# Optimization experiments

Hardware: AMD Instinct MI355X
Metric: run time of the kernel (lower is better)

## Reference

```python
import jax, jax.numpy as jnp
import numpy as np

N_NODES = 100000
N_EDGES = 3200000
G_EDGES = 1600000
D_FEAT = 256
K_CLUSTERS = 16
COLLAPSE_REG = 0.1


def setup_inputs() -> dict:
    key = jax.random.key(0)
    ks = jax.random.split(key, 12)
    inp = {
        'features': jax.random.normal(ks[0], (N_NODES, D_FEAT), dtype=jnp.float32),
        'W': jax.random.normal(ks[1], (D_FEAT, K_CLUSTERS), dtype=jnp.float32) / np.sqrt(D_FEAT),
        'b': jnp.zeros((K_CLUSTERS,), dtype=jnp.float32),
        'adj_src': jax.random.randint(ks[2], (N_EDGES,), 0, N_NODES, dtype=jnp.int32),
        'adj_dst': jax.random.randint(ks[3], (N_EDGES,), 0, N_NODES, dtype=jnp.int32),
        'adj_val': jax.random.uniform(ks[4], (N_EDGES,), dtype=jnp.float32),
        'g1_src': jax.random.randint(ks[5], (G_EDGES,), 0, N_NODES, dtype=jnp.int32),
        'g1_dst': jax.random.randint(ks[6], (G_EDGES,), 0, N_NODES, dtype=jnp.int32),
        'g1_val': jax.random.uniform(ks[7], (G_EDGES,), dtype=jnp.float32),
        'g2_src': jax.random.randint(ks[8], (G_EDGES,), 0, N_NODES, dtype=jnp.int32),
        'g2_dst': jax.random.randint(ks[9], (G_EDGES,), 0, N_NODES, dtype=jnp.int32),
        'g2_val': jax.random.uniform(ks[10], (G_EDGES,), dtype=jnp.float32),
        'lamda': 1,
    }
    return inp


def _spmm(src, dst, val, X, n):
    # (sparse A) @ X where A[src, dst] = val : out[i] = sum_j A[i,j] X[j]
    return jax.ops.segment_sum(val[:, None] * X[dst], src, num_segments=n)


def _col_degrees(src, dst, val, n):
    # tf.sparse.reduce_sum(A, axis=0): column sums
    return jax.ops.segment_sum(val, dst, num_segments=n)


def reference(features, W, b, adj_src, adj_dst, adj_val,
              g1_src, g1_dst, g1_val, g2_src, g2_dst, g2_val, lamda):
    n = features.shape[0]
    k = W.shape[1]
    # soft cluster assignments  [n, k]
    S = jax.nn.softmax(features @ W + b, axis=1)
    cluster_sizes = jnp.sum(S, axis=0)            # [k]
    S_pool = S / cluster_sizes                    # [n, k]

    # full-graph modularity
    deg = _col_degrees(adj_src, adj_dst, adj_val, n)  # [n]
    m = jnp.sum(deg)                                  # total edge weight
    AS = _spmm(adj_src, adj_dst, adj_val, S, n)       # [n, k]
    graph_pooled = AS.T @ S                           # [k, k]
    dS = deg @ S                                      # [k] = S^T deg
    normalizer = jnp.outer(dS, dS) / 2.0 / m          # [k, k]
    spectral_loss = -jnp.trace(graph_pooled - normalizer) / 2.0 / m

    # per-group modularity Q_g
    def group_Q(src, dst, val):
        gdeg = _col_degrees(src, dst, val, n)
        gm = jnp.sum(gdeg)
        safe_gm = jnp.where(gm > 0, gm, 1.0)
        gAS = _spmm(src, dst, val, S, n)
        g_pooled = gAS.T @ S
        gdS = gdeg @ S
        g_norm = jnp.outer(gdS, gdS) / 2.0 / safe_gm
        Qg = jnp.trace(g_pooled - g_norm) / 2.0 / m
        return jnp.where(gm > 0, Qg, 0.0), gm

    Q1, m1 = group_Q(g1_src, g1_dst, g1_val)
    Q2, m2 = group_Q(g2_src, g2_dst, g2_val)
    Q_min = jnp.minimum(Q1, Q2)
    g_edges_mean = (m1 + m2) / 2.0
    edge_ratio = m / (g_edges_mean + 1e-8)
    fairness_loss = edge_ratio * (-Q_min)

    collapse_loss = (jnp.linalg.norm(cluster_sizes) / n) * jnp.sqrt(jnp.float32(k)) - 1.0

    total_loss = spectral_loss + lamda * fairness_loss + COLLAPSE_REG * collapse_loss

    features_pooled = jax.nn.selu(S_pool.T @ features)  # [k, d]
    return features_pooled, S, total_loss
```

## Files before the change

### kernel.cpp

```cpp
#include <hip/hip_runtime.h>
#include <hip/hip_fp16.h>
#include <cstddef>


#define G1_MAX   1024
#define EGRID    2048
#define OFF_E    ((size_t)G1_MAX * 4112)
#define OFF_R    (OFF_E + (size_t)3 * 18 * EGRID)
#define OFF_G    (OFF_R + 4112)
#define OFF_H    (OFF_G + 64)

__global__ void __launch_bounds__(256)
k_rows(const float* __restrict__ F, const float* __restrict__ W,
       const float* __restrict__ b, float* __restrict__ S_out,
       __half* __restrict__ S_h, float* __restrict__ ws_P, int n, int n_tiles)
{
    __shared__ float Wt[16][260];
    __shared__ float rows[16][260];
    __shared__ float S_lds[16][17];
    __shared__ float cs_red[256];

    const int t = threadIdx.x;

    for (int idx = t; idx < 4096; idx += 256)
        Wt[idx & 15][idx >> 4] = W[idx];

    const float bk = b[t & 15];
    const int rl = t >> 4;
    const int kl = t & 15;
    const int kp = t & 15;
    const int cp = t >> 4;

    float4 P0 = {0,0,0,0}, P1 = {0,0,0,0}, P2 = {0,0,0,0}, P3 = {0,0,0,0};
    float cs_acc = 0.f;
    __syncthreads();

    for (int tile = blockIdx.x; tile < n_tiles; tile += gridDim.x) {
        const int row0 = tile << 4;
        const float4* F4 = (const float4*)(F + (size_t)row0 * 256);
        #pragma unroll
        for (int q = 0; q < 4; ++q) {
            int idx = t + (q << 8);
            int r = idx >> 6, dc = idx & 63;
            float4 v = {0.f, 0.f, 0.f, 0.f};
            if (row0 + r < n) v = F4[idx];
            *(float4*)&rows[r][dc << 2] = v;
        }
        __syncthreads();

        float acc = 0.f;
        #pragma unroll 8
        for (int dd = 0; dd < 64; ++dd) {
            float4 f4 = *(const float4*)&rows[rl][dd << 2];
            float4 w4 = *(const float4*)&Wt[kl][dd << 2];
            acc = fmaf(f4.x, w4.x, acc);
            acc = fmaf(f4.y, w4.y, acc);
            acc = fmaf(f4.z, w4.z, acc);
            acc = fmaf(f4.w, w4.w, acc);
        }
        acc += bk;

        float mx = acc;
        #pragma unroll
        for (int o = 8; o; o >>= 1) mx = fmaxf(mx, __shfl_xor(mx, o, 16));
        float ev = __expf(acc - mx);
        float sm = ev;
        #pragma unroll
        for (int o = 8; o; o >>= 1) sm += __shfl_xor(sm, o, 16);
        float sval = ev / sm;

        const bool valid = (row0 + rl) < n;
        if (valid) {
            S_out[(((size_t)(row0 + rl)) << 4) + kl] = sval;
            S_h[(((size_t)(row0 + rl)) << 4) + kl] = __float2half(sval);
            cs_acc += sval;
        }
        S_lds[rl][kl] = valid ? sval : 0.f;
        __syncthreads();

        #pragma unroll 4
        for (int r = 0; r < 16; ++r) {
            float sv = S_lds[r][kp];
            const float* rp = &rows[r][cp << 4];
            float4 f0 = *(const float4*)&rp[0];
            float4 f1 = *(const float4*)&rp[4];
            float4 f2 = *(const float4*)&rp[8];
            float4 f3 = *(const float4*)&rp[12];
            P0.x = fmaf(sv, f0.x, P0.x); P0.y = fmaf(sv, f0.y, P0.y);
            P0.z = fmaf(sv, f0.z, P0.z); P0.w = fmaf(sv, f0.w, P0.w);
            P1.x = fmaf(sv, f1.x, P1.x); P1.y = fmaf(sv, f1.y, P1.y);
            P1.z = fmaf(sv, f1.z, P1.z); P1.w = fmaf(sv, f1.w, P1.w);
            P2.x = fmaf(sv, f2.x, P2.x); P2.y = fmaf(sv, f2.y, P2.y);
            P2.z = fmaf(sv, f2.z, P2.z); P2.w = fmaf(sv, f2.w, P2.w);
            P3.x = fmaf(sv, f3.x, P3.x); P3.y = fmaf(sv, f3.y, P3.y);
            P3.z = fmaf(sv, f3.z, P3.z); P3.w = fmaf(sv, f3.w, P3.w);
        }
        __syncthreads();
    }

    {
        float* dst = ws_P + (size_t)blockIdx.x * 4112 + kp * 256 + (cp << 4);
        *(float4*)&dst[0]  = P0;
        *(float4*)&dst[4]  = P1;
        *(float4*)&dst[8]  = P2;
        *(float4*)&dst[12] = P3;
    }
    cs_red[t] = cs_acc;
    __syncthreads();
    if (t < 16) {
        float ssum = 0.f;
        #pragma unroll
        for (int i = 0; i < 16; ++i) ssum += cs_red[t + (i << 4)];
        ws_P[(size_t)blockIdx.x * 4112 + 4096 + t] = ssum;
    }
}

#define NSEG 16
__global__ void __launch_bounds__(256)
k_reduce(const float* __restrict__ ws_P, float* __restrict__ ws_red, int nb)
{
    const int seg  = blockIdx.x & (NSEG - 1);
    const int jblk = blockIdx.x / NSEG;
    const int idx  = jblk * 256 + threadIdx.x;
    if (idx >= 4112) return;
    const int chunk = (nb + NSEG - 1) / NSEG;
    const int b0 = seg * chunk;
    const int b1 = min(nb, b0 + chunk);
    float s = 0.f;
    for (int bb = b0; bb < b1; ++bb)
        s += ws_P[(size_t)bb * 4112 + idx];
    atomicAdd(&ws_red[idx], s);
}

__global__ void __launch_bounds__(256)
k_edges_all(const int* __restrict__ src0, const int* __restrict__ dst0,
            const float* __restrict__ val0, int n0,
            const int* __restrict__ src1, const int* __restrict__ dst1,
            const float* __restrict__ val1, int n1,
            const int* __restrict__ src2, const int* __restrict__ dst2,
            const float* __restrict__ val2, int n2,
            const __half* __restrict__ S_h, float* __restrict__ ws_e,
            int b0, int b1)
{
    int g, bb, nblk;
    const int* src; const int* dst; const float* val; int nE;
    if ((int)blockIdx.x < b0)      { g = 0; bb = blockIdx.x;          nblk = b0; src = src0; dst = dst0; val = val0; nE = n0; }
    else if ((int)blockIdx.x < b1) { g = 1; bb = blockIdx.x - b0;     nblk = b1 - b0; src = src1; dst = dst1; val = val1; nE = n1; }
    else                           { g = 2; bb = blockIdx.x - b1;     nblk = gridDim.x - b1; src = src2; dst = dst2; val = val2; nE = n2; }

    float m_acc = 0.f, tr_acc = 0.f;
    float gds[16];
    #pragma unroll
    for (int k = 0; k < 16; ++k) gds[k] = 0.f;

    const int nv = nE >> 2;
    const int stride = nblk * 256;
    for (int i = bb * 256 + threadIdx.x; i < nv; i += stride) {
        int4   s4 = ((const int4*)src)[i];
        int4   d4 = ((const int4*)dst)[i];
        float4 v4 = ((const float4*)val)[i];
        #pragma unroll
        for (int e = 0; e < 4; ++e) {
            int   si = (&s4.x)[e];
            int   di = (&d4.x)[e];
            float v  = (&v4.x)[e];
            uint4 sa = *(const uint4*)(S_h + ((size_t)si << 4));
            uint4 sb = *(const uint4*)(S_h + ((size_t)si << 4) + 8);
            uint4 da = *(const uint4*)(S_h + ((size_t)di << 4));
            uint4 db = *(const uint4*)(S_h + ((size_t)di << 4) + 8);
            float dot = 0.f;
            float dv[16];
            #pragma unroll
            for (int j = 0; j < 4; ++j) {
                float2 as = __half22float2(*(const __half2*)(&(&sa.x)[j]));
                float2 ad = __half22float2(*(const __half2*)(&(&da.x)[j]));
                float2 bs = __half22float2(*(const __half2*)(&(&sb.x)[j]));
                float2 bd = __half22float2(*(const __half2*)(&(&db.x)[j]));
                dot = fmaf(as.x, ad.x, dot); dot = fmaf(as.y, ad.y, dot);
                dot = fmaf(bs.x, bd.x, dot); dot = fmaf(bs.y, bd.y, dot);
                dv[2*j]     = ad.x; dv[2*j + 1] = ad.y;
                dv[8 + 2*j] = bd.x; dv[9 + 2*j] = bd.y;
            }
            m_acc += v;
            tr_acc = fmaf(v, dot, tr_acc);
            #pragma unroll
            for (int k = 0; k < 16; ++k) gds[k] = fmaf(v, dv[k], gds[k]);
        }
    }

    #pragma unroll
    for (int o = 32; o; o >>= 1) {
        m_acc  += __shfl_xor(m_acc, o);
        tr_acc += __shfl_xor(tr_acc, o);
        #pragma unroll
        for (int k = 0; k < 16; ++k) gds[k] += __shfl_xor(gds[k], o);
    }
    __shared__ float wred[4][18];
    const int wid = threadIdx.x >> 6, lane = threadIdx.x & 63;
    if (lane == 0) {
        wred[wid][0] = m_acc; wred[wid][1] = tr_acc;
        #pragma unroll
        for (int k = 0; k < 16; ++k) wred[wid][2 + k] = gds[k];
    }
    __syncthreads();
    if (threadIdx.x < 18) {
        float s = wred[0][threadIdx.x] + wred[1][threadIdx.x]
                + wred[2][threadIdx.x] + wred[3][threadIdx.x];
        ws_e[(size_t)g * 18 * EGRID + (size_t)threadIdx.x * EGRID + bb] = s;
    }
}

__global__ void __launch_bounds__(256)
k_ereduce(const float* __restrict__ ws_e, float* __restrict__ G54,
          int g0, int g1, int g2)
{
    const int p = blockIdx.x;
    const int g = p / 18, slot = p % 18;
    int grids[3] = {g0, g1, g2};
    const int gb = grids[g];
    const float* base = ws_e + (size_t)g * 18 * EGRID + (size_t)slot * EGRID;

    const int t = threadIdx.x;
    float s = 0.f;
    for (int bb = t; bb < gb; bb += 256) s += base[bb];
    #pragma unroll
    for (int o = 32; o; o >>= 1) s += __shfl_xor(s, o);

    __shared__ float wr[4];
    if ((t & 63) == 0) wr[t >> 6] = s;
    __syncthreads();
    if (t == 0) G54[p] = wr[0] + wr[1] + wr[2] + wr[3];
}

__global__ void __launch_bounds__(256)
k_final(const float* __restrict__ ws_red, const float* __restrict__ G54,
        const void* __restrict__ lamda_ptr, float* __restrict__ out, int n)
{
    __shared__ float G[54];
    const int t = threadIdx.x;
    if (t < 54) G[t] = G54[t];
    __syncthreads();

    const float* P  = ws_red;
    const float* cs = ws_red + 4096;

    const float scale = 1.0507009873554805f;
    const float alpha = 1.6732632423543772f;
    for (int idx = t; idx < 4096; idx += 256) {
        int k = idx >> 8;
        float x = P[idx] / cs[k];
        float y = x > 0.f ? scale * x : scale * alpha * (expf(x) - 1.f);
        out[idx] = y;
    }

    if (t == 0) {
        int   li = *(const int*)lamda_ptr;
        float lf = *(const float*)lamda_ptr;
        float lamda = (li > -100000 && li < 100000) ? (float)li : lf;

        float m = G[0], trA = G[1];
        float ds2 = 0.f;
        for (int k = 0; k < 16; ++k) ds2 += G[2 + k] * G[2 + k];
        float spectral = -(trA - ds2 / (2.f * m)) / (2.f * m);

        float Q[2], gm[2];
        for (int g = 0; g < 2; ++g) {
            const float* Gg = G + 18 * (g + 1);
            float mg = Gg[0], trg = Gg[1];
            float gds2 = 0.f;
            for (int k = 0; k < 16; ++k) gds2 += Gg[2 + k] * Gg[2 + k];
            float safe = mg > 0.f ? mg : 1.f;
            float q = (trg - gds2 / (2.f * safe)) / (2.f * m);
            Q[g]  = mg > 0.f ? q : 0.f;
            gm[g] = mg;
        }
        float Qmin = fminf(Q[0], Q[1]);
        float gmean = 0.5f * (gm[0] + gm[1]);
        float fairness = (m / (gmean + 1e-8f)) * (-Qmin);

        float csn = 0.f;
        for (int k = 0; k < 16; ++k) csn += cs[k] * cs[k];
        float collapse = (sqrtf(csn) / (float)n) * 4.f - 1.f;

        out[4096 + (size_t)n * 16] = spectral + lamda * fairness + 0.1f * collapse;
    }
}

extern "C" void kernel_launch(void* const* d_in, const int* in_sizes, int n_in,
                              void* d_out, int out_size, void* d_ws, size_t ws_size,
                              hipStream_t stream)
{
    const float* F       = (const float*)d_in[0];
    const float* W       = (const float*)d_in[1];
    const float* b       = (const float*)d_in[2];
    const int*   adj_src = (const int*)d_in[3];
    const int*   adj_dst = (const int*)d_in[4];
    const float* adj_val = (const float*)d_in[5];
    const int*   g1_src  = (const int*)d_in[6];
    const int*   g1_dst  = (const int*)d_in[7];
    const float* g1_val  = (const float*)d_in[8];
    const int*   g2_src  = (const int*)d_in[9];
    const int*   g2_dst  = (const int*)d_in[10];
    const float* g2_val  = (const float*)d_in[11];
    const void*  lamda_p = d_in[12];

    const int n  = in_sizes[0] / 256;
    const int nE = in_sizes[3];
    const int n1 = in_sizes[6];
    const int n2 = in_sizes[9];

    float*  out   = (float*)d_out;
    float*  S_out = out + 4096;
    float*  ws    = (float*)d_ws;
    float*  ws_e  = ws + OFF_E;
    float*  ws_r  = ws + OFF_R;
    float*  ws_g  = ws + OFF_G;
    __half* ws_h  = (__half*)(ws + OFF_H);

    const int n_tiles = (n + 15) >> 4;
    int grid1 = n_tiles < G1_MAX ? n_tiles : G1_MAX;

    k_rows<<<grid1, 256, 0, stream>>>(F, W, b, S_out, ws_h, ws, n, n_tiles);

    hipMemsetAsync(ws_r, 0, 4112 * sizeof(float), stream);
    k_reduce<<<17 * NSEG, 256, 0, stream>>>(ws, ws_r, grid1);

    auto eg = [](int ne) { int g = (ne / 4 + 255) / 256; if (g < 1) g = 1; return g < EGRID ? g : EGRID; };
    const int b0 = eg(nE), b1g = eg(n1), b2g = eg(n2);
    k_edges_all<<<b0 + b1g + b2g, 256, 0, stream>>>(
        adj_src, adj_dst, adj_val, nE,
        g1_src, g1_dst, g1_val, n1,
        g2_src, g2_dst, g2_val, n2,
        ws_h, ws_e, b0, b0 + b1g);

    k_ereduce<<<54, 256, 0, stream>>>(ws_e, ws_g, b0, b1g, b2g);
    k_final<<<1, 256, 0, stream>>>(ws_r, ws_g, lamda_p, out, n);
}
```

Measured before the change: 173.0 us.

## Store S as FP8 and compute degree-weighted sums via scatter plus dense pass

The soft assignment matrix S is now stored in an FP8 e4m3 copy (16 bytes per row instead of 32), which halves the bytes gathered per edge endpoint. The per-edge deg@S accumulation of 16 values is replaced by an atomic scatter of edge weights into per-node column degrees. A new dense kernel then multiplies those degrees by the full-precision S, and each edge thread processes 8 edges with batched gathers. This trades register-heavy per-edge FMAs and reductions for global float atomics and an extra memset. FP8 precision in the trace term is a risk to accuracy.

```diff
diff --git a/kernel.cpp b/kernel.cpp
--- a/kernel.cpp
+++ b/kernel.cpp
@@ -1,19 +1,73 @@
 #include <hip/hip_runtime.h>
-#include <hip/hip_fp16.h>
 #include <cstddef>
+#include <cstdint>
 
 
 #define G1_MAX   1024
 #define EGRID    2048
-#define OFF_E    ((size_t)G1_MAX * 4112)
-#define OFF_R    (OFF_E + (size_t)3 * 18 * EGRID)
+#define NSEG     16
+#define OFF_E    0
+#define SZ_E     (3 * 18 * EGRID)
+#define OFF_R    (OFF_E + SZ_E)
 #define OFF_G    (OFF_R + 4112)
-#define OFF_H    (OFF_G + 64)
+#define OFF_W    (OFF_G + 64)
+
+#if __has_builtin(__builtin_amdgcn_cvt_pk_f32_fp8)
+#define HW_FP8 1
+#endif
+
+__device__ __forceinline__ unsigned f32_to_e4m3(float f)
+{
+    unsigned bits = __float_as_uint(f);
+    unsigned s = bits >> 31;
+    int e32 = (int)((bits >> 23) & 255);
+    unsigned m23 = bits & 0x7FFFFF;
+    int e = e32 - 120;
+    unsigned out;
+    if (e32 == 0) out = 0;
+    else if (e <= 0) {
+        float av = fabsf(f);
+        int q = (int)(av * 512.0f + 0.5f);
+        out = (unsigned)q;
+    } else if (e > 15) out = (15u << 3) | 6u;
+    else {
+        unsigned m3 = (m23 + 0x80000u) >> 20;
+        if (m3 == 8u) { m3 = 0u; ++e; if (e > 15) { e = 15; m3 = 6u; } }
+        out = ((unsigned)e << 3) | m3;
+    }
+    return out | (s << 7);
+}
+
+__device__ __forceinline__ float dot_rows(uint4 ra, uint4 rb, const float* lut)
+{
+    float dot = 0.f;
+#ifdef HW_FP8
+    #pragma unroll
+    for (int j = 0; j < 4; ++j) {
+        unsigned ua = (&ra.x)[j], ub = (&rb.x)[j];
+        auto a0 = __builtin_amdgcn_cvt_pk_f32_fp8(ua, false);
+        auto a1 = __builtin_amdgcn_cvt_pk_f32_fp8(ua, true);
+        auto b0 = __builtin_amdgcn_cvt_pk_f32_fp8(ub, false);
+        auto b1 = __builtin_amdgcn_cvt_pk_f32_fp8(ub, true);
+        dot = fmaf(a0[0], b0[0], dot); dot = fmaf(a0[1], b0[1], dot);
+        dot = fmaf(a1[0], b1[0], dot); dot = fmaf(a1[1], b1[1], dot);
+    }
+#else
+    #pragma unroll
+    for (int j = 0; j < 4; ++j) {
+        unsigned ua = (&ra.x)[j], ub = (&rb.x)[j];
+        #pragma unroll
+        for (int q = 0; q < 4; ++q)
+            dot = fmaf(lut[(ua >> (8*q)) & 255], lut[(ub >> (8*q)) & 255], dot);
+    }
+#endif
+    return dot;
+}
 
 __global__ void __launch_bounds__(256)
 k_rows(const float* __restrict__ F, const float* __restrict__ W,
        const float* __restrict__ b, float* __restrict__ S_out,
-       __half* __restrict__ S_h, float* __restrict__ ws_P, int n, int n_tiles)
+       unsigned* __restrict__ S_f8, float* __restrict__ ws_P, int n, int n_tiles)
 {
     __shared__ float Wt[16][260];
     __shared__ float rows[16][260];
@@ -72,11 +126,22 @@
         const bool valid = (row0 + rl) < n;
         if (valid) {
             S_out[(((size_t)(row0 + rl)) << 4) + kl] = sval;
-            S_h[(((size_t)(row0 + rl)) << 4) + kl] = __float2half(sval);
             cs_acc += sval;
         }
         S_lds[rl][kl] = valid ? sval : 0.f;
         __syncthreads();
+
+        if (t < 64) {
+            int r = t >> 2, c = t & 3;
+            int row = row0 + r;
+            if (row < n) {
+                unsigned u = f32_to_e4m3(S_lds[r][4*c])
+                           | (f32_to_e4m3(S_lds[r][4*c+1]) << 8)
+                           | (f32_to_e4m3(S_lds[r][4*c+2]) << 16)
+                           | (f32_to_e4m3(S_lds[r][4*c+3]) << 24);
+                S_f8[((size_t)row << 2) + c] = u;
+            }
+        }
 
         #pragma unroll 4
         for (int r = 0; r < 16; ++r) {
@@ -115,7 +180,6 @@
     }
 }
 
-#define NSEG 16
 __global__ void __launch_bounds__(256)
 k_reduce(const float* __restrict__ ws_P, float* __restrict__ ws_red, int nb)
 {
@@ -132,100 +196,154 @@
     atomicAdd(&ws_red[idx], s);
 }
 
+__global__ void __launch_bounds__(256, 4)
+k_edge(const int* __restrict__ src0, const int* __restrict__ dst0,
+       const float* __restrict__ val0, int n0,
+       const int* __restrict__ src1, const int* __restrict__ dst1,
+       const float* __restrict__ val1, int n1,
+       const int* __restrict__ src2, const int* __restrict__ dst2,
+       const float* __restrict__ val2, int n2,
+       const unsigned* __restrict__ S8, float* __restrict__ w,
+       float* __restrict__ ws_e, int b0, int b1, int n_nodes)
+{
+#ifndef HW_FP8
+    __shared__ float lut[256];
+    if (threadIdx.x < 256) {
+        int i = threadIdx.x;
+        int e_ = (i >> 3) & 15, m_ = i & 7, s_ = i >> 7;
+        float v = e_ ? ldexpf((float)(8 + m_), e_ - 10) : ldexpf((float)m_, -9);
+        lut[i] = s_ ? -v : v;
+    }
+    __syncthreads();
+    const float* lutp = lut;
+#else
+    const float* lutp = nullptr;
+#endif
+
+    int g, bb, nblk, nE;
+    const int* src; const int* dst; const float* val;
+    if ((int)blockIdx.x < b0)      { g = 0; bb = blockIdx.x;      nblk = b0;             src = src0; dst = dst0; val = val0; nE = n0; }
+    else if ((int)blockIdx.x < b1) { g = 1; bb = blockIdx.x - b0; nblk = b1 - b0;        src = src1; dst = dst1; val = val1; nE = n1; }
+    else                           { g = 2; bb = blockIdx.x - b1; nblk = gridDim.x - b1; src = src2; dst = dst2; val = val2; nE = n2; }
+
+    float* wg = w + (size_t)g * n_nodes;
+    float tr = 0.f;
+
+    const int nv = nE >> 3;
+    const int4*   s4 = (const int4*)src;
+    const int4*   d4 = (const int4*)dst;
+    const float4* v4 = (const float4*)val;
+    const int stride = nblk * 256;
+
+    for (int i = bb * 256 + threadIdx.x; i < nv; i += stride) {
+        int4   sa = s4[2*i], sb = s4[2*i+1];
+        int4   da = d4[2*i], db = d4[2*i+1];
+        float4 va = v4[2*i], vb = v4[2*i+1];
+        int   is[8] = {sa.x, sa.y, sa.z, sa.w, sb.x, sb.y, sb.z, sb.w};
+        int   id[8] = {da.x, da.y, da.z, da.w, db.x, db.y, db.z, db.w};
+        float vv[8] = {va.x, va.y, va.z, va.w, vb.x, vb.y, vb.z, vb.w};
+        uint4 rs[8], rd[8];
+        #pragma unroll
+        for (int e = 0; e < 8; ++e) {
+            rs[e] = *(const uint4*)(S8 + ((size_t)is[e] << 2));
+            rd[e] = *(const uint4*)(S8 + ((size_t)id[e] << 2));
+        }
+        #pragma unroll
+        for (int e = 0; e < 8; ++e) {
+            float dot = dot_rows(rs[e], rd[e], lutp);
+            tr = fmaf(vv[e], dot, tr);
+            atomicAdd(&wg[id[e]], vv[e]);
+        }
+    }
+
+    if (bb == 0) {
+        int e = (nv << 3) + threadIdx.x;
+        if (e < nE) {
+            int si = src[e], di = dst[e];
+            float v = val[e];
+            uint4 ra = *(const uint4*)(S8 + ((size_t)si << 2));
+            uint4 rb = *(const uint4*)(S8 + ((size_t)di << 2));
+            tr = fmaf(v, dot_rows(ra, rb, lutp), tr);
+            atomicAdd(&wg[di], v);
+        }
+    }
+
+    #pragma unroll
+    for (int o = 32; o; o >>= 1) tr += __shfl_xor(tr, o);
+    __shared__ float wred[4];
+    if ((threadIdx.x & 63) == 0) wred[threadIdx.x >> 6] = tr;
+    __syncthreads();
+    if (threadIdx.x == 0)
+        ws_e[((size_t)g * 18 + 1) * EGRID + bb] = wred[0] + wred[1] + wred[2] + wred[3];
+}
+
 __global__ void __launch_bounds__(256)
-k_edges_all(const int* __restrict__ src0, const int* __restrict__ dst0,
-            const float* __restrict__ val0, int n0,
-            const int* __restrict__ src1, const int* __restrict__ dst1,
-            const float* __restrict__ val1, int n1,
-            const int* __restrict__ src2, const int* __restrict__ dst2,
-            const float* __restrict__ val2, int n2,
-            const __half* __restrict__ S_h, float* __restrict__ ws_e,
-            int b0, int b1)
-{
-    int g, bb, nblk;
-    const int* src; const int* dst; const float* val; int nE;
-    if ((int)blockIdx.x < b0)      { g = 0; bb = blockIdx.x;          nblk = b0; src = src0; dst = dst0; val = val0; nE = n0; }
-    else if ((int)blockIdx.x < b1) { g = 1; bb = blockIdx.x - b0;     nblk = b1 - b0; src = src1; dst = dst1; val = val1; nE = n1; }
-    else                           { g = 2; bb = blockIdx.x - b1;     nblk = gridDim.x - b1; src = src2; dst = dst2; val = val2; nE = n2; }
-
-    float m_acc = 0.f, tr_acc = 0.f;
-    float gds[16];
-    #pragma unroll
-    for (int k = 0; k < 16; ++k) gds[k] = 0.f;
-
-    const int nv = nE >> 2;
-    const int stride = nblk * 256;
-    for (int i = bb * 256 + threadIdx.x; i < nv; i += stride) {
-        int4   s4 = ((const int4*)src)[i];
-        int4   d4 = ((const int4*)dst)[i];
-        float4 v4 = ((const float4*)val)[i];
-        #pragma unroll
-        for (int e = 0; e < 4; ++e) {
-            int   si = (&s4.x)[e];
-            int   di = (&d4.x)[e];
-            float v  = (&v4.x)[e];
-            uint4 sa = *(const uint4*)(S_h + ((size_t)si << 4));
-            uint4 sb = *(const uint4*)(S_h + ((size_t)si << 4) + 8);
-            uint4 da = *(const uint4*)(S_h + ((size_t)di << 4));
-            uint4 db = *(const uint4*)(S_h + ((size_t)di << 4) + 8);
-            float dot = 0.f;
-            float dv[16];
+k_dense(const float* __restrict__ S, const float* __restrict__ w,
+        float* __restrict__ ws_e, int n)
+{
+    const int t = threadIdx.x;
+    const int i = blockIdx.x * 256 + t;
+    float m[3] = {0.f, 0.f, 0.f};
+    float gd[3][16];
+    #pragma unroll
+    for (int g = 0; g < 3; ++g)
+        #pragma unroll
+        for (int k = 0; k < 16; ++k) gd[g][k] = 0.f;
+
+    if (i < n) {
+        float w0 = w[i], w1 = w[n + i], w2 = w[2*n + i];
+        m[0] = w0; m[1] = w1; m[2] = w2;
+        const float4* Sr = (const float4*)(S + ((size_t)i << 4));
+        #pragma unroll
+        for (int j = 0; j < 4; ++j) {
+            float4 sv = Sr[j];
+            gd[0][4*j]   = w0*sv.x; gd[0][4*j+1] = w0*sv.y;
+            gd[0][4*j+2] = w0*sv.z; gd[0][4*j+3] = w0*sv.w;
+            gd[1][4*j]   = w1*sv.x; gd[1][4*j+1] = w1*sv.y;
+            gd[1][4*j+2] = w1*sv.z; gd[1][4*j+3] = w1*sv.w;
+            gd[2][4*j]   = w2*sv.x; gd[2][4*j+1] = w2*sv.y;
+            gd[2][4*j+2] = w2*sv.z; gd[2][4*j+3] = w2*sv.w;
+        }
+    }
+
+    #pragma unroll
+    for (int o = 32; o; o >>= 1) {
+        #pragma unroll
+        for (int g = 0; g < 3; ++g) {
+            m[g] += __shfl_xor(m[g], o);
             #pragma unroll
-            for (int j = 0; j < 4; ++j) {
-                float2 as = __half22float2(*(const __half2*)(&(&sa.x)[j]));
-                float2 ad = __half22float2(*(const __half2*)(&(&da.x)[j]));
-                float2 bs = __half22float2(*(const __half2*)(&(&sb.x)[j]));
-                float2 bd = __half22float2(*(const __half2*)(&(&db.x)[j]));
-                dot = fmaf(as.x, ad.x, dot); dot = fmaf(as.y, ad.y, dot);
-                dot = fmaf(bs.x, bd.x, dot); dot = fmaf(bs.y, bd.y, dot);
-                dv[2*j]     = ad.x; dv[2*j + 1] = ad.y;
-                dv[8 + 2*j] = bd.x; dv[9 + 2*j] = bd.y;
-            }
-            m_acc += v;
-            tr_acc = fmaf(v, dot, tr_acc);
+            for (int k = 0; k < 16; ++k) gd[g][k] += __shfl_xor(gd[g][k], o);
+        }
+    }
+    __shared__ float wr[4][51];
+    const int wid = t >> 6;
+    if ((t & 63) == 0) {
+        #pragma unroll
+        for (int g = 0; g < 3; ++g) {
+            wr[wid][g*17] = m[g];
             #pragma unroll
-            for (int k = 0; k < 16; ++k) gds[k] = fmaf(v, dv[k], gds[k]);
-        }
-    }
-
-    #pragma unroll
-    for (int o = 32; o; o >>= 1) {
-        m_acc  += __shfl_xor(m_acc, o);
-        tr_acc += __shfl_xor(tr_acc, o);
-        #pragma unroll
-        for (int k = 0; k < 16; ++k) gds[k] += __shfl_xor(gds[k], o);
-    }
-    __shared__ float wred[4][18];
-    const int wid = threadIdx.x >> 6, lane = threadIdx.x & 63;
-    if (lane == 0) {
-        wred[wid][0] = m_acc; wred[wid][1] = tr_acc;
-        #pragma unroll
-        for (int k = 0; k < 16; ++k) wred[wid][2 + k] = gds[k];
-    }
-    __syncthreads();
-    if (threadIdx.x < 18) {
-        float s = wred[0][threadIdx.x] + wred[1][threadIdx.x]
-                + wred[2][threadIdx.x] + wred[3][threadIdx.x];
-        ws_e[(size_t)g * 18 * EGRID + (size_t)threadIdx.x * EGRID + bb] = s;
+            for (int k = 0; k < 16; ++k) wr[wid][g*17 + 1 + k] = gd[g][k];
+        }
+    }
+    __syncthreads();
+    if (t < 51) {
+        float s = wr[0][t] + wr[1][t] + wr[2][t] + wr[3][t];
+        int g = t / 17, q = t % 17;
+        int slot = (q == 0) ? 0 : (q + 1);
+        ws_e[((size_t)g * 18 + slot) * EGRID + blockIdx.x] = s;
     }
 }
 
 __global__ void __launch_bounds__(256)
-k_ereduce(const float* __restrict__ ws_e, float* __restrict__ G54,
-          int g0, int g1, int g2)
+k_ereduce(const float* __restrict__ ws_e, float* __restrict__ G54)
 {
     const int p = blockIdx.x;
-    const int g = p / 18, slot = p % 18;
-    int grids[3] = {g0, g1, g2};
-    const int gb = grids[g];
-    const float* base = ws_e + (size_t)g * 18 * EGRID + (size_t)slot * EGRID;
-
+    const float* base = ws_e + (size_t)p * EGRID;
     const int t = threadIdx.x;
     float s = 0.f;
-    for (int bb = t; bb < gb; bb += 256) s += base[bb];
+    for (int bb = t; bb < EGRID; bb += 256) s += base[bb];
     #pragma unroll
     for (int o = 32; o; o >>= 1) s += __shfl_xor(s, o);
-
     __shared__ float wr[4];
     if ((t & 63) == 0) wr[t >> 6] = s;
     __syncthreads();
@@ -309,30 +427,42 @@
     const int n1 = in_sizes[6];
     const int n2 = in_sizes[9];
 
-    float*  out   = (float*)d_out;
-    float*  S_out = out + 4096;
-    float*  ws    = (float*)d_ws;
-    float*  ws_e  = ws + OFF_E;
-    float*  ws_r  = ws + OFF_R;
-    float*  ws_g  = ws + OFF_G;
-    __half* ws_h  = (__half*)(ws + OFF_H);
+    float* out   = (float*)d_out;
+    float* S_out = out + 4096;
+
+    float* ws   = (float*)d_ws;
+    float* ws_e = ws + OFF_E;
+    float* ws_r = ws + OFF_R;
+    float* ws_g = ws + OFF_G;
+    float* w    = ws + OFF_W;
+    const size_t off_f8 = (size_t)OFF_W + (size_t)3 * n;
+    unsigned* S8 = (unsigned*)(ws + off_f8);
+    const size_t off_p = off_f8 + (size_t)n * 4;
+    float* ws_P = ws + off_p;
 
     const int n_tiles = (n + 15) >> 4;
+    long avail = ((long)(ws_size / 4) - (long)off_p) / 4112;
     int grid1 = n_tiles < G1_MAX ? n_tiles : G1_MAX;
-
-    k_rows<<<grid1, 256, 0, stream>>>(F, W, b, S_out, ws_h, ws, n, n_tiles);
-
+    if (avail < grid1) grid1 = (int)avail;
+    if (grid1 < 1) grid1 = 1;
+
+    hipMemsetAsync(ws_e, 0, SZ_E * sizeof(float), stream);
     hipMemsetAsync(ws_r, 0, 4112 * sizeof(float), stream);
-    k_reduce<<<17 * NSEG, 256, 0, stream>>>(ws, ws_r, grid1);
-
-    auto eg = [](int ne) { int g = (ne / 4 + 255) / 256; if (g < 1) g = 1; return g < EGRID ? g : EGRID; };
+    hipMemsetAsync(w, 0, (size_t)3 * n * sizeof(float), stream);
+
+    k_rows<<<grid1, 256, 0, stream>>>(F, W, b, S_out, S8, ws_P, n, n_tiles);
+    k_reduce<<<17 * NSEG, 256, 0, stream>>>(ws_P, ws_r, grid1);
+
+    auto eg = [](int ne) { int g = (ne / 8 + 255) / 256; if (g < 1) g = 1;
+                           return g < EGRID ? g : EGRID; };
     const int b0 = eg(nE), b1g = eg(n1), b2g = eg(n2);
-    k_edges_all<<<b0 + b1g + b2g, 256, 0, stream>>>(
+    k_edge<<<b0 + b1g + b2g, 256, 0, stream>>>(
         adj_src, adj_dst, adj_val, nE,
         g1_src, g1_dst, g1_val, n1,
         g2_src, g2_dst, g2_val, n2,
-        ws_h, ws_e, b0, b0 + b1g);
-
-    k_ereduce<<<54, 256, 0, stream>>>(ws_e, ws_g, b0, b1g, b2g);
+        S8, w, ws_e, b0, b0 + b1g, n);
+
+    k_dense<<<(n + 255) / 256, 256, 0, stream>>>(S_out, w, ws_e, n);
+    k_ereduce<<<54, 256, 0, stream>>>(ws_e, ws_g);
     k_final<<<1, 256, 0, stream>>>(ws_r, ws_g, lamda_p, out, n);
 }
```

Result: slower. 442.7 us (+155.9%).
